# Kernel optimization log

Measured on AMD Instinct MI355X. Metric: run time of the kernel, lower is better.

Reference implementation:

```python
import jax, jax.numpy as jnp
import numpy as np

IN_F, OUT_F, RANK = 4096, 4096, 1024
B, S = 4, 2048


def soft_threshold24(w):
    """Soft-threshold 2:4 sparsification along the last dim.
    For each group of 4, the two smallest-magnitude entries are zeroed and the
    kept entries are shrunk by the threshold (2nd-smallest magnitude)."""
    g = w.reshape(-1, 4)
    m = jnp.abs(g)
    t = jnp.sort(m, axis=-1)[:, 1:2]  # largest pruned magnitude per group
    sp = jnp.sign(g) * jnp.maximum(m - t, 0.0)
    return sp.reshape(w.shape)


def fake_fp8_mm(a, b):
    """FP8-simulated GEMM: fp16 operands, fp32 accumulate/output (matches fake_fp8_mm)."""
    return jnp.matmul(a.astype(jnp.float16), b.astype(jnp.float16),
                      preferred_element_type=jnp.float32)


def setup_inputs() -> dict:
    key = jax.random.key(0)
    k1, k2, k3 = jax.random.split(key, 3)
    x = jax.random.normal(k1, (B, S, IN_F), dtype=jnp.float32)
    std_a = (2.0 / (IN_F + RANK)) ** 0.5   # xavier_normal for (in_features, rank)
    std_b = (2.0 / (OUT_F + RANK)) ** 0.5  # xavier_normal for (out_features, rank)
    weight_A = jax.random.normal(k2, (IN_F, RANK), dtype=jnp.float32) * std_a
    weight_B = jax.random.normal(k3, (OUT_F, RANK), dtype=jnp.float32) * std_b
    bias = jnp.zeros((OUT_F,), dtype=jnp.float32)
    scale_A = jnp.ones((), dtype=jnp.float32)  # sparse_init_scale buffer
    scale_B = jnp.ones((), dtype=jnp.float32)
    return {"x": x, "weight_A": weight_A, "weight_B": weight_B, "bias": bias,
            "scale_A": scale_A, "scale_B": scale_B}


def reference(x, weight_A, weight_B, bias, scale_A, scale_B):
    # sparse low-rank factors
    wa = soft_threshold24(weight_A) * scale_A  # (in, rank)
    wb = soft_threshold24(weight_B) * scale_B  # (out, rank)
    lead = x.shape[:-1]
    xf = x.reshape(-1, x.shape[-1])            # (T, in)
    x_proj = fake_fp8_mm(xf, wa)               # (T, rank) == x @ A_sparse
    out = fake_fp8_mm(x_proj, wb.T) + bias     # (T, out) == x_proj @ B_sparse^T + b
    return out.reshape(*lead, OUT_F)
```

## Files before the change

kernel.cpp:

```cpp
#include <hip/hip_runtime.h>

#define IN_FEAT 4096
#define OUT_FEAT 4096
#define RANK 1024
#define TOK 8192

typedef _Float16 f16x8 __attribute__((ext_vector_type(8)));
typedef _Float16 f16x4 __attribute__((ext_vector_type(4)));
typedef float f32x4 __attribute__((ext_vector_type(4)));

#define GLD_LDS16(g, l)                                                         \
  __builtin_amdgcn_global_load_lds(                                             \
      (__attribute__((address_space(1))) const void*)(g),                       \
      (__attribute__((address_space(3))) void*)(l), 16, 0, 0)

#define MIDBAR()                                        \
  __builtin_amdgcn_s_barrier();                         \
  asm volatile("s_waitcnt lgkmcnt(0)" ::: "memory")
#define ENDBAR() __builtin_amdgcn_s_barrier()


__device__ __forceinline__ void soft24(const float4 g, float s,
                                       float& r0, float& r1, float& r2, float& r3) {
  const float m0 = fabsf(g.x), m1 = fabsf(g.y), m2 = fabsf(g.z), m3 = fabsf(g.w);
  const float lo1 = fminf(m0, m1), hi1 = fmaxf(m0, m1);
  const float lo2 = fminf(m2, m3), hi2 = fmaxf(m2, m3);
  const float t = fminf(fmaxf(lo1, lo2), fminf(hi1, hi2));
  r0 = copysignf(fmaxf(m0 - t, 0.0f), g.x) * s;
  r1 = copysignf(fmaxf(m1 - t, 0.0f), g.y) * s;
  r2 = copysignf(fmaxf(m2 - t, 0.0f), g.z) * s;
  r3 = copysignf(fmaxf(m3 - t, 0.0f), g.w) * s;
}

__global__ __launch_bounds__(256) void sparsify_A_kernel(
    const float* __restrict__ wA, const float* __restrict__ scaleA,
    _Float16* __restrict__ waT) {
  const int idx = blockIdx.x * 256 + threadIdx.x;
  const int i = idx & (IN_FEAT - 1);
  const int jg = idx >> 12;
  const float4 g = *reinterpret_cast<const float4*>(wA + (size_t)i * RANK + jg * 4);
  const float s = scaleA[0];
  float r0, r1, r2, r3;
  soft24(g, s, r0, r1, r2, r3);
  const size_t base = (size_t)(jg * 4) * IN_FEAT + i;
  waT[base] = (_Float16)r0;
  waT[base + IN_FEAT] = (_Float16)r1;
  waT[base + 2 * IN_FEAT] = (_Float16)r2;
  waT[base + 3 * IN_FEAT] = (_Float16)r3;
}

__global__ __launch_bounds__(256) void sparsify_B_kernel(
    const float* __restrict__ wB, const float* __restrict__ scaleB,
    _Float16* __restrict__ wbs) {
  const int idx = blockIdx.x * 256 + threadIdx.x;
  const float4 g = *reinterpret_cast<const float4*>(wB + (size_t)idx * 4);
  const float s = scaleB[0];
  float r0, r1, r2, r3;
  soft24(g, s, r0, r1, r2, r3);
  f16x4 h;
  h[0] = (_Float16)r0; h[1] = (_Float16)r1; h[2] = (_Float16)r2; h[3] = (_Float16)r3;
  *reinterpret_cast<f16x4*>(wbs + (size_t)idx * 4) = h;
}

__global__ __launch_bounds__(256) void cast_x_kernel(
    const float* __restrict__ x, _Float16* __restrict__ x16) {
  const size_t i = ((size_t)blockIdx.x * 256 + threadIdx.x) * 8;
  const float4 f0 = *reinterpret_cast<const float4*>(x + i);
  const float4 f1 = *reinterpret_cast<const float4*>(x + i + 4);
  f16x8 h;
  h[0] = (_Float16)f0.x; h[1] = (_Float16)f0.y;
  h[2] = (_Float16)f0.z; h[3] = (_Float16)f0.w;
  h[4] = (_Float16)f1.x; h[5] = (_Float16)f1.y;
  h[6] = (_Float16)f1.z; h[7] = (_Float16)f1.w;
  *reinterpret_cast<f16x8*>(x16 + i) = h;
}

template <int N, int K, bool A_F32, bool OUT_F16>
__global__ __launch_bounds__(256, 4) void gemm128(
    const void* __restrict__ Av, const _Float16* __restrict__ Bh,
    void* __restrict__ Cv, const float* __restrict__ bias) {
  __shared__ __attribute__((aligned(128))) char lds[32768];
  char* ldsA = lds;
  char* ldsB = lds + 16384;

  const int tid = threadIdx.x;
  const int lane = tid & 63;
  const int w = tid >> 6;
  const int wrow = (w >> 1) * 64;
  const int wcol = (w & 1) * 64;

  constexpr int GX = N / 128;
  const int nwg = GX * (TOK / 128);
  const int l = blockIdx.y * GX + blockIdx.x;
  const int wg = (l & 7) * (nwg >> 3) + (l >> 3);
  const int brow = (wg / GX) * 128;
  const int bcol = (wg % GX) * 128;

  f32x4 acc[4][4] = {};

  for (int k0 = 0; k0 < K; k0 += 64) {
    __syncthreads();
#pragma unroll
    for (int it = 0; it < 4; ++it) {
      const int c = it * 256 + tid;
      const int row = c >> 3;
      const int u = c & 7;
      const _Float16* gsrc =
          Bh + (size_t)(bcol + row) * K + k0 + ((u ^ (row & 7)) << 3);
      GLD_LDS16(gsrc, ldsB + c * 16);
    }
    if constexpr (A_F32) {
      const float* Af = (const float*)Av;
#pragma unroll
      for (int it = 0; it < 4; ++it) {
        const int c = it * 256 + tid;
        const int row = c >> 3;
        const int u = c & 7;
        const float* gsrc = Af + (size_t)(brow + row) * K + k0 + (u << 3);
        const float4 f0 = *reinterpret_cast<const float4*>(gsrc);
        const float4 f1 = *reinterpret_cast<const float4*>(gsrc + 4);
        f16x8 h;
        h[0] = (_Float16)f0.x; h[1] = (_Float16)f0.y;
        h[2] = (_Float16)f0.z; h[3] = (_Float16)f0.w;
        h[4] = (_Float16)f1.x; h[5] = (_Float16)f1.y;
        h[6] = (_Float16)f1.z; h[7] = (_Float16)f1.w;
        *reinterpret_cast<f16x8*>(ldsA + row * 128 + ((u ^ (row & 7)) << 4)) = h;
      }
    } else {
      const _Float16* Ah = (const _Float16*)Av;
#pragma unroll
      for (int it = 0; it < 4; ++it) {
        const int c = it * 256 + tid;
        const int row = c >> 3;
        const int u = c & 7;
        const _Float16* gsrc =
            Ah + (size_t)(brow + row) * K + k0 + ((u ^ (row & 7)) << 3);
        GLD_LDS16(gsrc, ldsA + c * 16);
      }
    }
    __syncthreads();
#pragma unroll
    for (int kk = 0; kk < 2; ++kk) {
      f16x8 af[4], bf[4];
#pragma unroll
      for (int m = 0; m < 4; ++m) {
        const int row = wrow + m * 16 + (lane & 15);
        const int u = (kk * 4 + (lane >> 4)) ^ (row & 7);
        af[m] = *reinterpret_cast<const f16x8*>(ldsA + row * 128 + u * 16);
      }
#pragma unroll
      for (int n = 0; n < 4; ++n) {
        const int row = wcol + n * 16 + (lane & 15);
        const int u = (kk * 4 + (lane >> 4)) ^ (row & 7);
        bf[n] = *reinterpret_cast<const f16x8*>(ldsB + row * 128 + u * 16);
      }
#pragma unroll
      for (int m = 0; m < 4; ++m)
#pragma unroll
        for (int n = 0; n < 4; ++n)
          acc[m][n] =
              __builtin_amdgcn_mfma_f32_16x16x32_f16(af[m], bf[n], acc[m][n], 0, 0, 0);
    }
  }

  const int r4 = (lane >> 4) * 4;
  const int cl = lane & 15;
  if constexpr (OUT_F16) {
    _Float16* C = (_Float16*)Cv;
#pragma unroll
    for (int m = 0; m < 4; ++m)
#pragma unroll
      for (int n = 0; n < 4; ++n)
#pragma unroll
        for (int j = 0; j < 4; ++j) {
          const int rr = brow + wrow + m * 16 + r4 + j;
          const int cc = bcol + wcol + n * 16 + cl;
          C[(size_t)rr * N + cc] = (_Float16)acc[m][n][j];
        }
  } else {
    float* C = (float*)Cv;
#pragma unroll
    for (int n = 0; n < 4; ++n) {
      const int cc = bcol + wcol + n * 16 + cl;
      const float bv = bias[cc];
#pragma unroll
      for (int m = 0; m < 4; ++m)
#pragma unroll
        for (int j = 0; j < 4; ++j) {
          const int rr = brow + wrow + m * 16 + r4 + j;
          C[(size_t)rr * N + cc] = acc[m][n][j] + bv;
        }
    }
  }
}

template <int M, int N, int K>
__global__ __launch_bounds__(512, 2) void gemm1_m(
    const _Float16* __restrict__ A, const _Float16* __restrict__ B,
    _Float16* __restrict__ C) {
  extern __shared__ char lds[];

  const int tid = threadIdx.x;
  const int lane = tid & 63;
  const int w = tid >> 6;
  const int wr = w >> 2;
  const int wc = w & 3;
  const int l15 = lane & 15;
  const int ubase = lane >> 4;

  constexpr int GX = N / 256;
  constexpr int NWG = GX * (M / 128);
  const int l = blockIdx.y * GX + blockIdx.x;
  const int wg = (l & 7) * (NWG >> 3) + (l >> 3);
  const int brow = (wg / GX) * 128;
  const int bcol = (wg % GX) * 256;

  f32x4 acc[4][4] = {};
  f16x8 af[4][2], bf[4][2];

  auto stageA = [&](int kof, int slot) {
#pragma unroll
    for (int r = 0; r < 2; ++r) {
      const int c = r * 512 + tid;
      const int row = c >> 3;
      const int u = c & 7;
      GLD_LDS16(A + (size_t)(brow + row) * K + kof + ((u ^ (row & 7)) << 3),
                lds + slot * 16384 + c * 16);
    }
  };
  auto stageB = [&](int kof, int slot) {
#pragma unroll
    for (int r = 0; r < 4; ++r) {
      const int c = r * 512 + tid;
      const int row = c >> 3;
      const int u = c & 7;
      GLD_LDS16(B + (size_t)(bcol + row) * K + kof + ((u ^ (row & 7)) << 3),
                lds + 49152 + slot * 32768 + c * 16);
    }
  };

  constexpr int NT = K / 64;

  stageA(0, 0);
  stageB(0, 0);
  stageA(64, 1);
  stageB(64, 1);
  asm volatile("s_waitcnt vmcnt(6)" ::: "memory");
  __builtin_amdgcn_s_barrier();

  int slot = 0;
  for (int t = 0; t < NT; ++t) {
#pragma unroll
    for (int i = 0; i < 4; ++i)
#pragma unroll
      for (int ks = 0; ks < 2; ++ks) {
        const int row = wr * 64 + i * 16 + l15;
        const int u = (ks * 4 + ubase) ^ (row & 7);
        af[i][ks] =
            *reinterpret_cast<const f16x8*>(lds + slot * 16384 + row * 128 + u * 16);
      }
#pragma unroll
    for (int j = 0; j < 4; ++j)
#pragma unroll
      for (int ks = 0; ks < 2; ++ks) {
        const int row = wc * 64 + j * 16 + l15;
        const int u = (ks * 4 + ubase) ^ (row & 7);
        bf[j][ks] = *reinterpret_cast<const f16x8*>(lds + 49152 + slot * 32768 +
                                                    row * 128 + u * 16);
      }
    if (t + 2 < NT) {
      int s2 = slot + 2;
      if (s2 >= 3) s2 -= 3;
      stageA((t + 2) * 64, s2);
      stageB((t + 2) * 64, s2);
      asm volatile("s_waitcnt vmcnt(6)" ::: "memory");
    } else if (t + 2 == NT) {
      asm volatile("s_waitcnt vmcnt(0)" ::: "memory");
    }
    MIDBAR();
    __builtin_amdgcn_s_setprio(1);
#pragma unroll
    for (int ks = 0; ks < 2; ++ks)
#pragma unroll
      for (int i = 0; i < 4; ++i)
#pragma unroll
        for (int j = 0; j < 4; ++j)
          acc[i][j] = __builtin_amdgcn_mfma_f32_16x16x32_f16(
              bf[j][ks], af[i][ks], acc[i][j], 0, 0, 0);
    __builtin_amdgcn_s_setprio(0);
    ENDBAR();
    ++slot;
    if (slot == 3) slot = 0;
  }

  const int r4 = (lane >> 4) * 4;
#pragma unroll
  for (int m = 0; m < 4; ++m)
#pragma unroll
    for (int n = 0; n < 4; ++n) {
      const int rr = brow + wr * 64 + m * 16 + l15;
      const int cc = bcol + wc * 64 + n * 16 + r4;
      f16x4 h;
#pragma unroll
      for (int j = 0; j < 4; ++j) h[j] = (_Float16)acc[m][n][j];
      *reinterpret_cast<f16x4*>(C + (size_t)rr * N + cc) = h;
    }
}

#define AOFF(s, h) (((s) * 2 + (h)) * 16384)
#define BOFF(s, h) (65536 + ((s) * 2 + (h)) * 16384)

template <int M, int N, int K>
__global__ __launch_bounds__(512, 2) void gemm2_m(
    const _Float16* __restrict__ A, const _Float16* __restrict__ B,
    float* __restrict__ C, const float* __restrict__ bias) {
  extern __shared__ char lds[];

  const int tid = threadIdx.x;
  const int lane = tid & 63;
  const int w = tid >> 6;
  const int wr = w >> 2;
  const int wc = w & 3;
  const int l15 = lane & 15;
  const int ubase = lane >> 4;

  constexpr int GX = N / 256;
  constexpr int NWG = GX * (M / 256);
  const int l = blockIdx.y * GX + blockIdx.x;
  const int wg = (l & 7) * (NWG >> 3) + (l >> 3);
  const int brow = (wg / GX) * 256;
  const int bcol = (wg % GX) * 256;

  const _Float16* Abase = A + (size_t)brow * K;
  const _Float16* Bbase = B + (size_t)bcol * K;

  auto stage = [&](const _Float16* srcBase, int rowOff, int kof, int ldsOff) {
#pragma unroll
    for (int r = 0; r < 2; ++r) {
      const int c = r * 512 + tid;
      const int row = c >> 3;
      const int u = c & 7;
      const _Float16* g =
          srcBase + (size_t)(rowOff + row) * K + kof + ((u ^ (row & 7)) << 3);
      GLD_LDS16(g, lds + ldsOff + c * 16);
    }
  };

  f32x4 acc[8][4] = {};
  f16x8 af[4][2], bf01[2][2], bf23[2][2];

#define LDA_GRP(SLOT, MBASE)                                                   \
  _Pragma("unroll") for (int i = 0; i < 4; ++i)                                \
  _Pragma("unroll") for (int ks = 0; ks < 2; ++ks) {                           \
    const int row = ((MBASE) + i) * 16 + l15;                                  \
    const int u = (ks * 4 + ubase) ^ (row & 7);                                \
    af[i][ks] = *reinterpret_cast<const f16x8*>(                               \
        lds + AOFF(SLOT, wr) + row * 128 + u * 16);                            \
  }
#define LDB_GRP(SLOT, NBASE, DST)                                              \
  _Pragma("unroll") for (int j = 0; j < 2; ++j)                                \
  _Pragma("unroll") for (int ks = 0; ks < 2; ++ks) {                           \
    const int row = (wc & 1) * 64 + ((NBASE) + j) * 16 + l15;                  \
    const int u = (ks * 4 + ubase) ^ (row & 7);                                \
    DST[j][ks] = *reinterpret_cast<const f16x8*>(                              \
        lds + BOFF(SLOT, wc >> 1) + row * 128 + u * 16);                       \
  }

#define MFMA32(MO)                                                             \
  __builtin_amdgcn_s_setprio(1);                                               \
  _Pragma("unroll") for (int ks = 0; ks < 2; ++ks)                             \
  _Pragma("unroll") for (int i = 0; i < 4; ++i)                                \
  _Pragma("unroll") for (int j = 0; j < 2; ++j) {                              \
    acc[(MO) + i][j] = __builtin_amdgcn_mfma_f32_16x16x32_f16(                 \
        bf01[j][ks], af[i][ks], acc[(MO) + i][j], 0, 0, 0);                    \
    acc[(MO) + i][2 + j] = __builtin_amdgcn_mfma_f32_16x16x32_f16(             \
        bf23[j][ks], af[i][ks], acc[(MO) + i][2 + j], 0, 0, 0);                \
  }                                                                            \
  __builtin_amdgcn_s_setprio(0);

  constexpr int NT = K / 64;

  stage(Abase, 0, 0, AOFF(0, 0));
  stage(Abase, 128, 0, AOFF(0, 1));
  stage(Bbase, 0, 0, BOFF(0, 0));
  stage(Bbase, 128, 0, BOFF(0, 1));
  stage(Bbase, 0, 64, BOFF(1, 0));
  stage(Bbase, 128, 64, BOFF(1, 1));
  asm volatile("s_waitcnt vmcnt(4)" ::: "memory");
  __builtin_amdgcn_s_barrier();

  for (int tt = 0; tt < NT; tt += 2) {
    const bool last = (tt + 2 >= NT);
    const int kof1 = tt * 64 + 64;
    const int kof2 = tt * 64 + 128;
    const int kof3 = tt * 64 + 192;

    LDA_GRP(0, 0);
    LDB_GRP(0, 0, bf01);
    LDB_GRP(0, 2, bf23);
    stage(Abase, 0, kof1, AOFF(1, 0));
    stage(Abase, 128, kof1, AOFF(1, 1));
    MIDBAR();
    MFMA32(0);
    ENDBAR();

    LDA_GRP(0, 4);
    if (!last) {
      stage(Bbase, 0, kof2, BOFF(0, 0));
      stage(Bbase, 128, kof2, BOFF(0, 1));
      asm volatile("s_waitcnt vmcnt(4)" ::: "memory");
    } else {
      asm volatile("s_waitcnt vmcnt(0)" ::: "memory");
    }
    MIDBAR();
    MFMA32(4);
    ENDBAR();

    LDA_GRP(1, 0);
    LDB_GRP(1, 0, bf01);
    LDB_GRP(1, 2, bf23);
    if (!last) {
      stage(Abase, 0, kof2, AOFF(0, 0));
      stage(Abase, 128, kof2, AOFF(0, 1));
    }
    MIDBAR();
    MFMA32(0);
    ENDBAR();

    LDA_GRP(1, 4);
    if (!last) {
      stage(Bbase, 0, kof3, BOFF(1, 0));
      stage(Bbase, 128, kof3, BOFF(1, 1));
      asm volatile("s_waitcnt vmcnt(4)" ::: "memory");
    }
    MIDBAR();
    MFMA32(4);
    ENDBAR();
  }

  const int r4 = (lane >> 4) * 4;
#pragma unroll
  for (int n = 0; n < 4; ++n) {
    const int cc = bcol + wc * 64 + n * 16 + r4;
    const f32x4 bv = *reinterpret_cast<const f32x4*>(bias + cc);
#pragma unroll
    for (int m = 0; m < 8; ++m) {
      const int rr = brow + wr * 128 + m * 16 + l15;
      f32x4 o = acc[m][n] + bv;
      *reinterpret_cast<f32x4*>(C + (size_t)rr * N + cc) = o;
    }
  }
}


extern "C" void kernel_launch(void* const* d_in, const int* in_sizes, int n_in,
                              void* d_out, int out_size, void* d_ws, size_t ws_size,
                              hipStream_t stream) {
  const float* x = (const float*)d_in[0];
  const float* wA = (const float*)d_in[1];
  const float* wB = (const float*)d_in[2];
  const float* bias = (const float*)d_in[3];
  const float* scaleA = (const float*)d_in[4];
  const float* scaleB = (const float*)d_in[5];
  float* out = (float*)d_out;

  char* ws = (char*)d_ws;
  _Float16* waT = (_Float16*)ws;
  _Float16* wbs = (_Float16*)(ws + (size_t)RANK * IN_FEAT * 2);
  _Float16* xp =
      (_Float16*)(ws + (size_t)RANK * IN_FEAT * 2 + (size_t)OUT_FEAT * RANK * 2);
  _Float16* x16 = (_Float16*)(ws + (size_t)RANK * IN_FEAT * 2 +
                              (size_t)OUT_FEAT * RANK * 2 + (size_t)TOK * RANK * 2);
  const size_t needed = (size_t)RANK * IN_FEAT * 2 + (size_t)OUT_FEAT * RANK * 2 +
                        (size_t)TOK * RANK * 2 + (size_t)TOK * IN_FEAT * 2;

  hipLaunchKernelGGL(sparsify_A_kernel, dim3((IN_FEAT * RANK / 4) / 256), dim3(256),
                     0, stream, wA, scaleA, waT);
  hipLaunchKernelGGL(sparsify_B_kernel, dim3((OUT_FEAT * RANK / 4) / 256), dim3(256),
                     0, stream, wB, scaleB, wbs);

  if (ws_size >= needed) {
    hipLaunchKernelGGL(cast_x_kernel, dim3((TOK * IN_FEAT / 8) / 256), dim3(256),
                       0, stream, x, x16);
    (void)hipFuncSetAttribute(
        reinterpret_cast<const void*>(&gemm1_m<TOK, RANK, IN_FEAT>),
        hipFuncAttributeMaxDynamicSharedMemorySize, 147456);
    hipLaunchKernelGGL((gemm1_m<TOK, RANK, IN_FEAT>),
                       dim3(RANK / 256, TOK / 128), dim3(512), 147456, stream,
                       x16, waT, xp);
  } else {
    hipLaunchKernelGGL((gemm128<RANK, IN_FEAT, true, true>),
                       dim3(RANK / 128, TOK / 128), dim3(256), 0, stream,
                       (const void*)x, waT, (void*)xp, nullptr);
  }

  (void)hipFuncSetAttribute(
      reinterpret_cast<const void*>(&gemm2_m<TOK, OUT_FEAT, RANK>),
      hipFuncAttributeMaxDynamicSharedMemorySize, 131072);
  hipLaunchKernelGGL((gemm2_m<TOK, OUT_FEAT, RANK>),
                     dim3(OUT_FEAT / 256, TOK / 256), dim3(512), 131072, stream,
                     xp, wbs, out, bias);
}
```

Measured before the change: 204.8 us.

## Fuse fp32-to-fp16 cast of x into first GEMM's A-tile staging

Removes the separate cast_x kernel and its fp16 copy of x. The first GEMM now loads fp32 x tiles into registers, converts them to fp16 and writes them to swizzled LDS one iteration ahead, while B keeps using direct global-to-LDS loads. The goal is to save the extra pass over x (a 128MB read plus a 64MB write) and one kernel launch. In exchange, each workgroup reads x as fp32 (twice the bytes, repeated across the 4 column blocks), register pressure rises, and waitcnt accounting becomes more complex.

```diff
diff --git a/kernel.cpp b/kernel.cpp
--- a/kernel.cpp
+++ b/kernel.cpp
@@ -60,19 +60,6 @@
   f16x4 h;
   h[0] = (_Float16)r0; h[1] = (_Float16)r1; h[2] = (_Float16)r2; h[3] = (_Float16)r3;
   *reinterpret_cast<f16x4*>(wbs + (size_t)idx * 4) = h;
-}
-
-__global__ __launch_bounds__(256) void cast_x_kernel(
-    const float* __restrict__ x, _Float16* __restrict__ x16) {
-  const size_t i = ((size_t)blockIdx.x * 256 + threadIdx.x) * 8;
-  const float4 f0 = *reinterpret_cast<const float4*>(x + i);
-  const float4 f1 = *reinterpret_cast<const float4*>(x + i + 4);
-  f16x8 h;
-  h[0] = (_Float16)f0.x; h[1] = (_Float16)f0.y;
-  h[2] = (_Float16)f0.z; h[3] = (_Float16)f0.w;
-  h[4] = (_Float16)f1.x; h[5] = (_Float16)f1.y;
-  h[6] = (_Float16)f1.z; h[7] = (_Float16)f1.w;
-  *reinterpret_cast<f16x8*>(x16 + i) = h;
 }
 
 template <int N, int K, bool A_F32, bool OUT_F16>
@@ -195,8 +182,8 @@
 }
 
 template <int M, int N, int K>
-__global__ __launch_bounds__(512, 2) void gemm1_m(
-    const _Float16* __restrict__ A, const _Float16* __restrict__ B,
+__global__ __launch_bounds__(512, 2) void gemm1_f(
+    const float* __restrict__ A, const _Float16* __restrict__ B,
     _Float16* __restrict__ C) {
   extern __shared__ char lds[];
 
@@ -218,15 +205,32 @@
   f32x4 acc[4][4] = {};
   f16x8 af[4][2], bf[4][2];
 
-  auto stageA = [&](int kof, int slot) {
-#pragma unroll
-    for (int r = 0; r < 2; ++r) {
-      const int c = r * 512 + tid;
-      const int row = c >> 3;
-      const int u = c & 7;
-      GLD_LDS16(A + (size_t)(brow + row) * K + kof + ((u ^ (row & 7)) << 3),
-                lds + slot * 16384 + c * 16);
-    }
+  const int ar0 = tid >> 3, au0 = tid & 7;
+  const int ar1 = (512 + tid) >> 3, au1 = tid & 7;
+  float4 a0l, a0h, a1l, a1h;
+
+  auto issueA = [&](int kof) {
+    const float* p0 = A + (size_t)(brow + ar0) * K + kof + au0 * 8;
+    const float* p1 = A + (size_t)(brow + ar1) * K + kof + au1 * 8;
+    a0l = *reinterpret_cast<const float4*>(p0);
+    a0h = *reinterpret_cast<const float4*>(p0 + 4);
+    a1l = *reinterpret_cast<const float4*>(p1);
+    a1h = *reinterpret_cast<const float4*>(p1 + 4);
+  };
+  auto writeA = [&](int slot) {
+    f16x8 h0, h1;
+    h0[0] = (_Float16)a0l.x; h0[1] = (_Float16)a0l.y;
+    h0[2] = (_Float16)a0l.z; h0[3] = (_Float16)a0l.w;
+    h0[4] = (_Float16)a0h.x; h0[5] = (_Float16)a0h.y;
+    h0[6] = (_Float16)a0h.z; h0[7] = (_Float16)a0h.w;
+    h1[0] = (_Float16)a1l.x; h1[1] = (_Float16)a1l.y;
+    h1[2] = (_Float16)a1l.z; h1[3] = (_Float16)a1l.w;
+    h1[4] = (_Float16)a1h.x; h1[5] = (_Float16)a1h.y;
+    h1[6] = (_Float16)a1h.z; h1[7] = (_Float16)a1h.w;
+    *reinterpret_cast<f16x8*>(lds + slot * 16384 + ar0 * 128 +
+                              ((au0 ^ (ar0 & 7)) << 4)) = h0;
+    *reinterpret_cast<f16x8*>(lds + slot * 16384 + ar1 * 128 +
+                              ((au1 ^ (ar1 & 7)) << 4)) = h1;
   };
   auto stageB = [&](int kof, int slot) {
 #pragma unroll
@@ -241,11 +245,14 @@
 
   constexpr int NT = K / 64;
 
-  stageA(0, 0);
+  issueA(0);
   stageB(0, 0);
-  stageA(64, 1);
+  asm volatile("s_waitcnt vmcnt(4)" ::: "memory");
+  writeA(0);
+  issueA(64);
   stageB(64, 1);
-  asm volatile("s_waitcnt vmcnt(6)" ::: "memory");
+  asm volatile("s_waitcnt vmcnt(8)" ::: "memory");
+  asm volatile("s_waitcnt lgkmcnt(0)" ::: "memory");
   __builtin_amdgcn_s_barrier();
 
   int slot = 0;
@@ -268,13 +275,18 @@
         bf[j][ks] = *reinterpret_cast<const f16x8*>(lds + 49152 + slot * 32768 +
                                                     row * 128 + u * 16);
       }
+    if (t + 1 < NT) {
+      int s1 = slot + 1;
+      if (s1 >= 3) s1 -= 3;
+      writeA(s1);
+    }
     if (t + 2 < NT) {
       int s2 = slot + 2;
       if (s2 >= 3) s2 -= 3;
-      stageA((t + 2) * 64, s2);
+      issueA((t + 2) * 64);
       stageB((t + 2) * 64, s2);
-      asm volatile("s_waitcnt vmcnt(6)" ::: "memory");
-    } else if (t + 2 == NT) {
+      asm volatile("s_waitcnt vmcnt(8)" ::: "memory");
+    } else {
       asm volatile("s_waitcnt vmcnt(0)" ::: "memory");
     }
     MIDBAR();
@@ -469,10 +481,8 @@
   _Float16* wbs = (_Float16*)(ws + (size_t)RANK * IN_FEAT * 2);
   _Float16* xp =
       (_Float16*)(ws + (size_t)RANK * IN_FEAT * 2 + (size_t)OUT_FEAT * RANK * 2);
-  _Float16* x16 = (_Float16*)(ws + (size_t)RANK * IN_FEAT * 2 +
-                              (size_t)OUT_FEAT * RANK * 2 + (size_t)TOK * RANK * 2);
   const size_t needed = (size_t)RANK * IN_FEAT * 2 + (size_t)OUT_FEAT * RANK * 2 +
-                        (size_t)TOK * RANK * 2 + (size_t)TOK * IN_FEAT * 2;
+                        (size_t)TOK * RANK * 2;
 
   hipLaunchKernelGGL(sparsify_A_kernel, dim3((IN_FEAT * RANK / 4) / 256), dim3(256),
                      0, stream, wA, scaleA, waT);
@@ -480,14 +490,12 @@
                      0, stream, wB, scaleB, wbs);
 
   if (ws_size >= needed) {
-    hipLaunchKernelGGL(cast_x_kernel, dim3((TOK * IN_FEAT / 8) / 256), dim3(256),
-                       0, stream, x, x16);
     (void)hipFuncSetAttribute(
-        reinterpret_cast<const void*>(&gemm1_m<TOK, RANK, IN_FEAT>),
+        reinterpret_cast<const void*>(&gemm1_f<TOK, RANK, IN_FEAT>),
         hipFuncAttributeMaxDynamicSharedMemorySize, 147456);
-    hipLaunchKernelGGL((gemm1_m<TOK, RANK, IN_FEAT>),
+    hipLaunchKernelGGL((gemm1_f<TOK, RANK, IN_FEAT>),
                        dim3(RANK / 256, TOK / 128), dim3(512), 147456, stream,
-                       x16, waT, xp);
+                       x, waT, xp);
   } else {
     hipLaunchKernelGGL((gemm128<RANK, IN_FEAT, true, true>),
                        dim3(RANK / 128, TOK / 128), dim3(256), 0, stream,
```

Measured after the change: 194.3 us. -5.1%, faster.
